# Kernel optimization log

Hardware: AMD Instinct MI355X
Metric: run time of the kernel (lower is better)

Reference implementation:

```python
import jax, jax.numpy as jnp
import numpy as np

N_NODES = 50000
N_EDGES = 262144
N_OCP = 32768
N_GRAPHS = 64
H = 128          # hidden_size
F_IN = 128       # node feature dim (== H for the stub GNN)
N_LABELS = 10


def _lin(key, fan_in, fan_out):
    return jax.random.normal(key, (fan_in, fan_out), jnp.float32) * (1.0 / float(np.sqrt(fan_in)))


def setup_inputs() -> dict:
    key = jax.random.key(0)
    ks = jax.random.split(key, 16)
    x = jax.random.normal(ks[0], (N_NODES, F_IN), jnp.float32)
    edge_index = jax.random.randint(ks[1], (2, N_EDGES), 0, N_NODES)
    batch_vec = jnp.sort(jax.random.randint(ks[2], (N_NODES,), 0, N_GRAPHS))
    y = jax.random.randint(ks[3], (N_GRAPHS,), 0, N_LABELS)
    params = {
        # stub GNN (get_node_reps): one GCN-style layer
        'W_self': _lin(ks[4], F_IN, H),
        'W_nbr': _lin(ks[5], F_IN, H),
        'b_gnn': jnp.zeros((H,), jnp.float32),
        # edge_action_rep_generator: Linear(2H,4H) ELU Linear(4H,2H) ELU Linear(2H,H)
        'Wr1': _lin(ks[6], 2 * H, 4 * H), 'br1': jnp.zeros((4 * H,), jnp.float32),
        'Wr2': _lin(ks[7], 4 * H, 2 * H), 'br2': jnp.zeros((2 * H,), jnp.float32),
        'Wr3': _lin(ks[8], 2 * H, H),     'br3': jnp.zeros((H,), jnp.float32),
        # edge_action_prob_generator: Linear(H,H) ELU Linear(H,num_labels)
        'Wp1': _lin(ks[9], H, H),         'bp1': jnp.zeros((H,), jnp.float32),
        'Wp2': _lin(ks[10], H, N_LABELS), 'bp2': jnp.zeros((N_LABELS,), jnp.float32),
    }
    return dict(x=x, edge_index=edge_index, batch_vec=batch_vec, y=y, n_ocp=N_OCP, **params)


def reference(x, edge_index, batch_vec, y, n_ocp,
              W_self, W_nbr, b_gnn,
              Wr1, br1, Wr2, br2, Wr3, br3,
              Wp1, bp1, Wp2, bp2):
    N = x.shape[0]
    G = y.shape[0]

    def get_node_reps(ei):
        # stub for self.model.get_node_reps: elu(x @ W_self + A @ (x @ W_nbr))
        msg = x[ei[0]] @ W_nbr                                   # [E', H]
        agg = jax.ops.segment_sum(msg, ei[1], num_segments=N)    # [N, H]
        return jax.nn.elu(x @ W_self + agg + b_gnn)

    ocp_edge_index = edge_index[:, :n_ocp]    # state == True edges
    ava_edge_index = edge_index[:, n_ocp:]    # state == False edges

    ava_node_reps = get_node_reps(edge_index) - get_node_reps(ocp_edge_index)  # [N, H]

    # gather per available edge + concat src/dst reps -> [E_ava, 2H]
    a = jnp.concatenate([ava_node_reps[ava_edge_index[0]],
                         ava_node_reps[ava_edge_index[1]]], axis=1)
    # edge_action_rep_generator
    a = jax.nn.elu(a @ Wr1 + br1)
    a = jax.nn.elu(a @ Wr2 + br2)
    a = a @ Wr3 + br3                                            # [E_ava, H]
    # edge_action_prob_generator
    h = jax.nn.elu(a @ Wp1 + bp1)
    logits = h @ Wp2 + bp2                                       # [E_ava, L]

    seg = batch_vec[ava_edge_index[0]]                           # graph id per ava edge
    y_edge = y[seg]                                              # target label per edge
    sel = jnp.take_along_axis(logits, y_edge[:, None], axis=1)[:, 0]  # gather(1, y)

    # segment-wise softmax over edges of each graph
    mx = jax.ops.segment_max(sel, seg, num_segments=G)
    ex = jnp.exp(sel - mx[seg])
    probs = ex / jax.ops.segment_sum(ex, seg, num_segments=G)[seg]    # [E_ava]

    # scatter_max: per-graph max prob and its argmax edge index
    pmax = jax.ops.segment_max(probs, seg, num_segments=G)            # [G]
    E = probs.shape[0]
    idx = jnp.where(probs == pmax[seg], jnp.arange(E), E)
    added_actions = jax.ops.segment_min(idx, seg, num_segments=G)     # [G]

    return probs, pmax, added_actions
```

## Files before the change

kernel.cpp:

```cpp
#include <hip/hip_runtime.h>

#define NN   50000
#define NNP  50048
#define NE   262144
#define NOCP 32768
#define EAVA (NE - NOCP)
#define NG   64
#define HD   128
#define CAP  48
#define CHNK 32768

typedef _Float16 f16x8 __attribute__((ext_vector_type(8)));
typedef _Float16 f16x2 __attribute__((ext_vector_type(2)));
typedef float f32x4 __attribute__((ext_vector_type(4)));

#define WAITVM12() asm volatile("s_waitcnt vmcnt(12)" ::: "memory")
#define WAITVM6()  asm volatile("s_waitcnt vmcnt(6)" ::: "memory")
#define WAITVM0()  asm volatile("s_waitcnt vmcnt(0)" ::: "memory")

__device__ __forceinline__ float elu_f(float v) { return v > 0.f ? v : (expf(v) - 1.f); }

__device__ __forceinline__ unsigned fenc(float f) {
  unsigned u = __float_as_uint(f);
  return (u & 0x80000000u) ? ~u : (u | 0x80000000u);
}
__device__ __forceinline__ float fdec(unsigned u) {
  return __uint_as_float((u & 0x80000000u) ? (u & 0x7fffffffu) : ~u);
}

__device__ __forceinline__ void dma16(const void* g, void* l) {
  __builtin_amdgcn_global_load_lds((const __attribute__((address_space(1))) unsigned int*)g,
                                   (__attribute__((address_space(3))) unsigned int*)l,
                                   16, 0, 0);
}

__global__ __launch_bounds__(256) void zero_i(int* __restrict__ p, int n) {
  for (int i = blockIdx.x * 256 + threadIdx.x; i < n; i += gridDim.x * 256) p[i] = 0;
}

__global__ void init_small(unsigned* mx_enc, float* denom, unsigned* pmax_enc, int* amin) {
  int t = threadIdx.x;
  if (t < NG) { mx_enc[t] = 0u; denom[t] = 0.f; pmax_enc[t] = 0u; amin[t] = EAVA; }
}

__global__ __launch_bounds__(256) void zero_tails(_Float16* __restrict__ base) {
  int t = blockIdx.x * 256 + threadIdx.x;
  if (t >= 6 * 768) return;
  int arr = t / 768, off = t % 768;
  f16x8 z = {};
  *(f16x8*)(base + (size_t)arr * NNP * HD + (size_t)NN * HD + (size_t)off * 8) = z;
}

__global__ __launch_bounds__(256) void bucket_kernel(const int* __restrict__ ei,
    int* __restrict__ cnt, int* __restrict__ bucket) {
  int e = blockIdx.x * 256 + threadIdx.x;
  if (e >= NE) return;
  int dst = ei[NE + e];
  int src = ei[e];
  int slot = atomicAdd(&cnt[dst], 1);
  if (slot < CAP)
    bucket[(size_t)dst * CAP + slot] = (int)((unsigned)src | (e < NOCP ? 0x80000000u : 0u));
}

__global__ __launch_bounds__(256) void gather_kernel(const float* __restrict__ x,
    const int* __restrict__ cnt, const int* __restrict__ bucket,
    _Float16* __restrict__ xsah, _Float16* __restrict__ xsal,
    _Float16* __restrict__ xsoh, _Float16* __restrict__ xsol) {
  int n = blockIdx.x * 4 + (threadIdx.x >> 6);
  if (n >= NN) return;
  int lane = threadIdx.x & 63;
  int c = cnt[n];
  if (c > CAP) c = CAP;
  float2 aall = make_float2(0.f, 0.f), aocp = aall;
  const int* bk = bucket + (size_t)n * CAP;
  for (int i0 = 0; i0 < c; i0 += 4) {
    int4 pk = *(const int4*)(bk + i0);
    bool m1 = (i0 + 1 < c), m2 = (i0 + 2 < c), m3 = (i0 + 3 < c);
    int r0 = pk.x & 0x7fffffff;
    int r1 = m1 ? (pk.y & 0x7fffffff) : 0;
    int r2 = m2 ? (pk.z & 0x7fffffff) : 0;
    int r3 = m3 ? (pk.w & 0x7fffffff) : 0;
    float2 v0 = *(const float2*)(x + (size_t)r0 * HD + lane * 2);
    float2 v1 = *(const float2*)(x + (size_t)r1 * HD + lane * 2);
    float2 v2 = *(const float2*)(x + (size_t)r2 * HD + lane * 2);
    float2 v3 = *(const float2*)(x + (size_t)r3 * HD + lane * 2);
    aall.x += v0.x; aall.y += v0.y;
    if (pk.x < 0) { aocp.x += v0.x; aocp.y += v0.y; }
    if (m1) { aall.x += v1.x; aall.y += v1.y; if (pk.y < 0) { aocp.x += v1.x; aocp.y += v1.y; } }
    if (m2) { aall.x += v2.x; aall.y += v2.y; if (pk.z < 0) { aocp.x += v2.x; aocp.y += v2.y; } }
    if (m3) { aall.x += v3.x; aall.y += v3.y; if (pk.w < 0) { aocp.x += v3.x; aocp.y += v3.y; } }
  }
  size_t o = (size_t)n * HD + lane * 2;
  _Float16 h0 = (_Float16)aall.x, h1 = (_Float16)aall.y;
  *(f16x2*)(xsah + o) = (f16x2){h0, h1};
  *(f16x2*)(xsal + o) = (f16x2){(_Float16)(aall.x - (float)h0), (_Float16)(aall.y - (float)h1)};
  _Float16 g0 = (_Float16)aocp.x, g1 = (_Float16)aocp.y;
  *(f16x2*)(xsoh + o) = (f16x2){g0, g1};
  *(f16x2*)(xsol + o) = (f16x2){(_Float16)(aocp.x - (float)g0), (_Float16)(aocp.y - (float)g1)};
}

__global__ __launch_bounds__(256) void split_x(const float* __restrict__ r,
    _Float16* __restrict__ rh, _Float16* __restrict__ rl) {
  int t = blockIdx.x * 256 + threadIdx.x;
  if (t >= NN * HD / 8) return;
  const float4* p = (const float4*)(r + (size_t)t * 8);
  float4 v0 = p[0], v1 = p[1];
  float vv[8] = {v0.x, v0.y, v0.z, v0.w, v1.x, v1.y, v1.z, v1.w};
  f16x8 hv, lv;
#pragma unroll
  for (int j = 0; j < 8; ++j) {
    _Float16 hh = (_Float16)vv[j];
    hv[j] = hh;
    lv[j] = (_Float16)(vv[j] - (float)hh);
  }
  *(f16x8*)(rh + (size_t)t * 8) = hv;
  *(f16x8*)(rl + (size_t)t * 8) = lv;
}

__global__ void pack_w2(const float* __restrict__ Wself, const float* __restrict__ Wnbr,
    _Float16* __restrict__ oh, _Float16* __restrict__ ol) {
  int chunk = blockIdx.x;
  int lane = threadIdx.x;
  int ns = chunk & 7, kt = chunk >> 3;
  int n = ns * 16 + (lane & 15);
  int k0 = kt * 32 + (lane >> 4) * 8;
  f16x8 hv, lv;
#pragma unroll
  for (int j = 0; j < 8; ++j) {
    int k = k0 + j;
    float v = (k < 128) ? Wself[(size_t)k * 128 + n] : Wnbr[(size_t)(k - 128) * 128 + n];
    _Float16 hh = (_Float16)v;
    hv[j] = hh;
    lv[j] = (_Float16)(v - (float)hh);
  }
  *(f16x8*)(oh + (size_t)chunk * 512 + lane * 8) = hv;
  *(f16x8*)(ol + (size_t)chunk * 512 + lane * 8) = lv;
}

__global__ void pack_w(const float* __restrict__ W, int K, int N,
    _Float16* __restrict__ oh, _Float16* __restrict__ ol) {
  int chunk = blockIdx.x;
  int lane = threadIdx.x;
  int NS = N >> 4;
  int ns = chunk % NS, kt = chunk / NS;
  int n = ns * 16 + (lane & 15);
  int k0 = kt * 32 + (lane >> 4) * 8;
  f16x8 hv, lv;
#pragma unroll
  for (int j = 0; j < 8; ++j) {
    float v = W[(size_t)(k0 + j) * N + n];
    _Float16 hh = (_Float16)v;
    hv[j] = hh;
    lv[j] = (_Float16)(v - (float)hh);
  }
  *(f16x8*)(oh + (size_t)chunk * 512 + lane * 8) = hv;
  *(f16x8*)(ol + (size_t)chunk * 512 + lane * 8) = lv;
}

__global__ void w34_kernel(const float* __restrict__ Wr3, const float* __restrict__ Wp1,
    const float* __restrict__ br3, const float* __restrict__ bp1,
    float* __restrict__ W34, float* __restrict__ b34) {
  int i = blockIdx.x, j = threadIdx.x;
  float s = 0.f;
  for (int k = 0; k < 128; ++k) s += Wr3[i * 128 + k] * Wp1[k * 128 + j];
  W34[i * 128 + j] = s;
  if (i == 0) {
    float t = bp1[j];
    for (int k = 0; k < 128; ++k) t += br3[k] * Wp1[k * 128 + j];
    b34[j] = t;
  }
}

template <int KT, int NS_B, int AMODE, int KT_NEXT, int NB>
__global__ __launch_bounds__(256) void gemm_ab(
    const _Float16* __restrict__ Ah, const _Float16* __restrict__ Al,
    const int* __restrict__ idx0, const int* __restrict__ idx1,
    const _Float16* __restrict__ Bh, const _Float16* __restrict__ Bl,
    const float* __restrict__ bias,
    _Float16* __restrict__ Oh, _Float16* __restrict__ Ol) {
  __shared__ char smem[73728] __attribute__((aligned(16)));
  float* sC = (float*)smem;

  const int tid = threadIdx.x;
  const int w = tid >> 6, lane = tid & 63;
  const int l16 = lane & 15, g16 = lane >> 4;
  const int f = blockIdx.x;
  const int r8 = f & 7;
  const int nb = (f >> 3) % NB;
  const int q8 = f / (8 * NB);
  const int bm = (q8 * 8 + r8) * 128, bn = nb * 64;
  const int w2r = w >> 1, w2c = w & 1;
  const int bmT = bm >> 4, bnS = bn >> 4;

  f32x4 acc[4][2];
#pragma unroll
  for (int i = 0; i < 4; ++i)
#pragma unroll
    for (int j = 0; j < 2; ++j) acc[i][j] = (f32x4)0.f;

  int i0a = 0, i0b = 0, i1a = 0, i1b = 0;
  if constexpr (AMODE == 1) {
    int rr0 = bm + w * 32 + l16;
    i0a = idx0[rr0]; i0b = idx0[rr0 + 16];
    i1a = idx1[rr0]; i1b = idx1[rr0 + 16];
  }

  auto STAGE = [&](int kt, int buf) {
    char* base = smem + buf * 24576;
    if constexpr (AMODE == 0) {
#pragma unroll
      for (int s = 0; s < 2; ++s) {
        int msub = w * 2 + s;
        size_t ch = (size_t)(bmT + msub) * KT + kt;
        dma16((const char*)Ah + ch * 1024 + lane * 16, base + msub * 1024);
        dma16((const char*)Al + ch * 1024 + lane * 16, base + 8192 + msub * 1024);
      }
    } else {
      int col = (kt & 3) * 32 + g16 * 8;
      int r0 = (kt < 4) ? i0a : i1a;
      int r1 = (kt < 4) ? i0b : i1b;
      dma16(Ah + (size_t)r0 * HD + col, base + (w * 2) * 1024);
      dma16(Al + (size_t)r0 * HD + col, base + 8192 + (w * 2) * 1024);
      dma16(Ah + (size_t)r1 * HD + col, base + (w * 2 + 1) * 1024);
      dma16(Al + (size_t)r1 * HD + col, base + 8192 + (w * 2 + 1) * 1024);
    }
    size_t chb = (size_t)kt * NS_B + bnS + w;
    dma16((const char*)Bh + chb * 1024 + lane * 16, base + 16384 + w * 1024);
    dma16((const char*)Bl + chb * 1024 + lane * 16, base + 20480 + w * 1024);
  };

  auto COMPUTE = [&](int buf) {
    const _Float16* sAh = (const _Float16*)(smem + buf * 24576);
    const _Float16* sAl = (const _Float16*)(smem + buf * 24576 + 8192);
    const _Float16* sBh = (const _Float16*)(smem + buf * 24576 + 16384);
    const _Float16* sBl = (const _Float16*)(smem + buf * 24576 + 20480);
    f16x8 ah[4], al[4];
#pragma unroll
    for (int mi = 0; mi < 4; ++mi) {
      ah[mi] = *(const f16x8*)(sAh + (w2r * 4 + mi) * 512 + lane * 8);
      al[mi] = *(const f16x8*)(sAl + (w2r * 4 + mi) * 512 + lane * 8);
    }
#pragma unroll
    for (int ni = 0; ni < 2; ++ni) {
      f16x8 bh = *(const f16x8*)(sBh + (w2c * 2 + ni) * 512 + lane * 8);
      f16x8 bl = *(const f16x8*)(sBl + (w2c * 2 + ni) * 512 + lane * 8);
#pragma unroll
      for (int mi = 0; mi < 4; ++mi) {
        acc[mi][ni] = __builtin_amdgcn_mfma_f32_16x16x32_f16(ah[mi], bh, acc[mi][ni], 0, 0, 0);
        acc[mi][ni] = __builtin_amdgcn_mfma_f32_16x16x32_f16(al[mi], bh, acc[mi][ni], 0, 0, 0);
        acc[mi][ni] = __builtin_amdgcn_mfma_f32_16x16x32_f16(ah[mi], bl, acc[mi][ni], 0, 0, 0);
      }
    }
  };

  STAGE(0, 0);
  STAGE(1, 1);
#pragma unroll
  for (int kt = 0; kt < KT; ++kt) {
    if (kt + 2 < KT) STAGE(kt + 2, (kt + 2) % 3);
    if (kt < KT - 2) WAITVM12();
    else if (kt == KT - 2) WAITVM6();
    else WAITVM0();
    __builtin_amdgcn_s_barrier();
    COMPUTE(kt % 3);
    __builtin_amdgcn_s_barrier();
  }

#pragma unroll
  for (int ni = 0; ni < 2; ++ni) {
    int colL = (w2c * 2 + ni) * 16 + l16;
    float bv = bias[bn + colL];
#pragma unroll
    for (int mi = 0; mi < 4; ++mi) {
      int rowb = w2r * 64 + mi * 16 + g16 * 4;
#pragma unroll
      for (int r = 0; r < 4; ++r)
        sC[(rowb + r) * 68 + colL] = elu_f(acc[mi][ni][r] + bv);
    }
  }
  __syncthreads();
  const int bnT32 = bn >> 5;
#pragma unroll
  for (int c = 0; c < 4; ++c) {
    int chunkid = w * 4 + c;
    int msub = chunkid >> 1, ktl = chunkid & 1;
    int m = msub * 16 + l16;
    int cb = ktl * 32 + g16 * 8;
    f16x8 hv, lv;
#pragma unroll
    for (int j = 0; j < 8; ++j) {
      float v = sC[m * 68 + cb + j];
      _Float16 hh = (_Float16)v;
      hv[j] = hh;
      lv[j] = (_Float16)(v - (float)hh);
    }
    size_t gchunk = (size_t)(bmT + msub) * KT_NEXT + (bnT32 + ktl);
    *(f16x8*)((char*)Oh + gchunk * 1024 + lane * 16) = hv;
    *(f16x8*)((char*)Ol + gchunk * 1024 + lane * 16) = lv;
  }
}

__global__ __launch_bounds__(64) void reps_direct(
    const _Float16* __restrict__ xh, const _Float16* __restrict__ xl,
    const _Float16* __restrict__ xsah, const _Float16* __restrict__ xsal,
    const _Float16* __restrict__ xsoh, const _Float16* __restrict__ xsol,
    const _Float16* __restrict__ Wsh, const _Float16* __restrict__ Wsl,
    const float* __restrict__ bias,
    _Float16* __restrict__ Oh, _Float16* __restrict__ Ol) {
  __shared__ float sC[64][68];
  const int lane = threadIdx.x;
  const int mt = blockIdx.x, nt = blockIdx.y;
  const int bm = mt * 64, bn = nt * 64;
  const int l16 = lane & 15, g16 = lane >> 4;

  f32x4 acc1[4][4], acc2[4][4];
#pragma unroll
  for (int i = 0; i < 4; ++i)
#pragma unroll
    for (int j = 0; j < 4; ++j) acc1[i][j] = (f32x4)0.f;

  auto CP3 = [&](f32x4 (*acc)[4], const f16x8* ah, const f16x8* al,
                 const f16x8* bh, const f16x8* bl) {
#pragma unroll
    for (int ni = 0; ni < 4; ++ni)
#pragma unroll
      for (int mi = 0; mi < 4; ++mi) {
        acc[mi][ni] = __builtin_amdgcn_mfma_f32_16x16x32_f16(ah[mi], bh[ni], acc[mi][ni], 0, 0, 0);
        acc[mi][ni] = __builtin_amdgcn_mfma_f32_16x16x32_f16(al[mi], bh[ni], acc[mi][ni], 0, 0, 0);
        acc[mi][ni] = __builtin_amdgcn_mfma_f32_16x16x32_f16(ah[mi], bl[ni], acc[mi][ni], 0, 0, 0);
      }
  };

#pragma unroll
  for (int kt = 0; kt < 4; ++kt) {
    f16x8 ah[4], al[4], bh[4], bl[4];
#pragma unroll
    for (int mi = 0; mi < 4; ++mi) {
      size_t off = (size_t)(bm + mi * 16 + l16) * HD + kt * 32 + g16 * 8;
      ah[mi] = *(const f16x8*)(xh + off);
      al[mi] = *(const f16x8*)(xl + off);
    }
#pragma unroll
    for (int ni = 0; ni < 4; ++ni) {
      size_t ch = (size_t)kt * 8 + nt * 4 + ni;
      bh[ni] = *(const f16x8*)(Wsh + ch * 512 + lane * 8);
      bl[ni] = *(const f16x8*)(Wsl + ch * 512 + lane * 8);
    }
    CP3(acc1, ah, al, bh, bl);
  }
#pragma unroll
  for (int i = 0; i < 4; ++i)
#pragma unroll
    for (int j = 0; j < 4; ++j) acc2[i][j] = acc1[i][j];

#pragma unroll
  for (int kt = 0; kt < 4; ++kt) {
    f16x8 aah[4], aal[4], aoh[4], aol[4], bh[4], bl[4];
#pragma unroll
    for (int mi = 0; mi < 4; ++mi) {
      size_t off = (size_t)(bm + mi * 16 + l16) * HD + kt * 32 + g16 * 8;
      aah[mi] = *(const f16x8*)(xsah + off);
      aal[mi] = *(const f16x8*)(xsal + off);
      aoh[mi] = *(const f16x8*)(xsoh + off);
      aol[mi] = *(const f16x8*)(xsol + off);
    }
#pragma unroll
    for (int ni = 0; ni < 4; ++ni) {
      size_t ch = (size_t)(kt + 4) * 8 + nt * 4 + ni;
      bh[ni] = *(const f16x8*)(Wsh + ch * 512 + lane * 8);
      bl[ni] = *(const f16x8*)(Wsl + ch * 512 + lane * 8);
    }
    CP3(acc1, aah, aal, bh, bl);
    CP3(acc2, aoh, aol, bh, bl);
  }

#pragma unroll
  for (int ni = 0; ni < 4; ++ni) {
    int colL = ni * 16 + l16;
    float bv = bias[bn + colL];
#pragma unroll
    for (int mi = 0; mi < 4; ++mi) {
      int rowb = mi * 16 + g16 * 4;
#pragma unroll
      for (int r = 0; r < 4; ++r)
        sC[rowb + r][colL] = elu_f(acc1[mi][ni][r] + bv) - elu_f(acc2[mi][ni][r] + bv);
    }
  }
  __syncthreads();
#pragma unroll
  for (int c = 0; c < 8; ++c) {
    int msub = c >> 1, ktl = c & 1;
    int m = msub * 16 + l16;
    int cb = ktl * 32 + g16 * 8;
    int grow = bm + m;
    if (grow < NN) {
      f16x8 hv, lv;
#pragma unroll
      for (int j = 0; j < 8; ++j) {
        float v = sC[m][cb + j];
        _Float16 hh = (_Float16)v;
        hv[j] = hh;
        lv[j] = (_Float16)(v - (float)hh);
      }
      *(f16x8*)(Oh + (size_t)grow * HD + bn + cb) = hv;
      *(f16x8*)(Ol + (size_t)grow * HD + bn + cb) = lv;
    }
  }
}

__global__ __launch_bounds__(256) void gemm3_sel(
    const _Float16* __restrict__ Ah, const _Float16* __restrict__ Al,
    const _Float16* __restrict__ Bh, const _Float16* __restrict__ Bl,
    const float* __restrict__ b34,
    const int* __restrict__ ei, const int* __restrict__ batchv, const int* __restrict__ yv,
    const float* __restrict__ Wp2, const float* __restrict__ bp2,
    float* __restrict__ sel, int* __restrict__ seg, int co) {
  __shared__ char smem[73728] __attribute__((aligned(16)));
  const int tid = threadIdx.x;
  const int w = tid >> 6, lane = tid & 63;
  const int l16 = lane & 15, g16 = lane >> 4;
  const int mt = blockIdx.x;

  f32x4 acc[8];
#pragma unroll
  for (int j = 0; j < 8; ++j) acc[j] = (f32x4)0.f;

  auto STAGE = [&](int kt, int buf) {
    char* base = smem + buf * 24576;
    size_t ch = (size_t)(mt * 4 + w) * 8 + kt;
    dma16((const char*)Ah + ch * 1024 + lane * 16, base + w * 1024);
    dma16((const char*)Al + ch * 1024 + lane * 16, base + 4096 + w * 1024);
#pragma unroll
    for (int s = 0; s < 2; ++s) {
      int nsub = w * 2 + s;
      size_t chb = (size_t)kt * 8 + nsub;
      dma16((const char*)Bh + chb * 1024 + lane * 16, base + 8192 + nsub * 1024);
      dma16((const char*)Bl + chb * 1024 + lane * 16, base + 16384 + nsub * 1024);
    }
  };

  auto COMPUTE = [&](int buf) {
    const _Float16* sAh = (const _Float16*)(smem + buf * 24576);
    const _Float16* sAl = (const _Float16*)(smem + buf * 24576 + 4096);
    const _Float16* sBh = (const _Float16*)(smem + buf * 24576 + 8192);
    const _Float16* sBl = (const _Float16*)(smem + buf * 24576 + 16384);
    f16x8 ah = *(const f16x8*)(sAh + w * 512 + lane * 8);
    f16x8 al = *(const f16x8*)(sAl + w * 512 + lane * 8);
#pragma unroll
    for (int ni = 0; ni < 8; ++ni) {
      f16x8 bh = *(const f16x8*)(sBh + ni * 512 + lane * 8);
      f16x8 bl = *(const f16x8*)(sBl + ni * 512 + lane * 8);
      acc[ni] = __builtin_amdgcn_mfma_f32_16x16x32_f16(ah, bh, acc[ni], 0, 0, 0);
      acc[ni] = __builtin_amdgcn_mfma_f32_16x16x32_f16(al, bh, acc[ni], 0, 0, 0);
      acc[ni] = __builtin_amdgcn_mfma_f32_16x16x32_f16(ah, bl, acc[ni], 0, 0, 0);
    }
  };

  STAGE(0, 0);
  STAGE(1, 1);
#pragma unroll
  for (int kt = 0; kt < 8; ++kt) {
    if (kt + 2 < 8) STAGE(kt + 2, (kt + 2) % 3);
    if (kt < 6) WAITVM12();
    else if (kt == 6) WAITVM6();
    else WAITVM0();
    __builtin_amdgcn_s_barrier();
    COMPUTE(kt % 3);
    __builtin_amdgcn_s_barrier();
  }

  float bb[8];
#pragma unroll
  for (int ni = 0; ni < 8; ++ni) bb[ni] = b34[ni * 16 + l16];

#pragma unroll
  for (int rr = 0; rr < 4; ++rr) {
    int row = w * 16 + g16 * 4 + rr;
    int e = co + mt * 64 + row;
    int s = ei[NOCP + e];
    int gg = batchv[s];
    int c = yv[gg];
    float a = 0.f;
#pragma unroll
    for (int ni = 0; ni < 8; ++ni)
      a += elu_f(acc[ni][rr] + bb[ni]) * Wp2[(ni * 16 + l16) * 10 + c];
    a += __shfl_xor(a, 1);
    a += __shfl_xor(a, 2);
    a += __shfl_xor(a, 4);
    a += __shfl_xor(a, 8);
    if (l16 == 0) { sel[e] = a + bp2[c]; seg[e] = gg; }
  }
}

__global__ __launch_bounds__(256) void segmax_sel(const float* __restrict__ sel,
    const int* __restrict__ seg, unsigned* __restrict__ mx_enc) {
  __shared__ unsigned sm[NG];
  int tid = threadIdx.x;
  if (tid < NG) sm[tid] = 0u;
  __syncthreads();
  for (int i = blockIdx.x * blockDim.x + tid; i < EAVA; i += gridDim.x * blockDim.x)
    atomicMax(&sm[seg[i]], fenc(sel[i]));
  __syncthreads();
  if (tid < NG) atomicMax(&mx_enc[tid], sm[tid]);
}

__global__ __launch_bounds__(256) void exden_kernel(const float* __restrict__ sel,
    const int* __restrict__ seg, const unsigned* __restrict__ mx_enc,
    float* __restrict__ denom, float* __restrict__ out_probs) {
  __shared__ float sd[NG];
  __shared__ float smx[NG];
  int tid = threadIdx.x;
  if (tid < NG) { smx[tid] = fdec(mx_enc[tid]); sd[tid] = 0.f; }
  __syncthreads();
  for (int i = blockIdx.x * blockDim.x + tid; i < EAVA; i += gridDim.x * blockDim.x) {
    int g = seg[i];
    float ex = expf(sel[i] - smx[g]);
    out_probs[i] = ex;
    atomicAdd(&sd[g], ex);
  }
  __syncthreads();
  if (tid < NG) atomicAdd(&denom[tid], sd[tid]);
}

__global__ __launch_bounds__(256) void probpmax_kernel(const int* __restrict__ seg,
    const float* __restrict__ denom, float* __restrict__ out_probs,
    unsigned* __restrict__ pmax_enc) {
  __shared__ float sden[NG];
  __shared__ unsigned sp[NG];
  int tid = threadIdx.x;
  if (tid < NG) { sden[tid] = denom[tid]; sp[tid] = 0u; }
  __syncthreads();
  for (int i = blockIdx.x * blockDim.x + tid; i < EAVA; i += gridDim.x * blockDim.x) {
    int g = seg[i];
    float p = out_probs[i] / sden[g];
    out_probs[i] = p;
    atomicMax(&sp[g], fenc(p));
  }
  __syncthreads();
  if (tid < NG) atomicMax(&pmax_enc[tid], sp[tid]);
}

__global__ __launch_bounds__(256) void argmin_kernel(const int* __restrict__ seg,
    const float* __restrict__ out_probs, const unsigned* __restrict__ pmax_enc,
    int* __restrict__ amin) {
  __shared__ float spm[NG];
  __shared__ int sa[NG];
  int tid = threadIdx.x;
  if (tid < NG) { spm[tid] = fdec(pmax_enc[tid]); sa[tid] = EAVA; }
  __syncthreads();
  for (int i = blockIdx.x * blockDim.x + tid; i < EAVA; i += gridDim.x * blockDim.x) {
    int g = seg[i];
    if (out_probs[i] == spm[g]) atomicMin(&sa[g], i);
  }
  __syncthreads();
  if (tid < NG) atomicMin(&amin[tid], sa[tid]);
}

__global__ void finalize_kernel(const unsigned* __restrict__ pmax_enc,
    const int* __restrict__ amin, float* __restrict__ out) {
  int g = threadIdx.x;
  if (g < NG) {
    out[EAVA + g] = fdec(pmax_enc[g]);
    out[EAVA + NG + g] = (float)amin[g];
  }
}

extern "C" void kernel_launch(void* const* d_in, const int* in_sizes, int n_in,
                              void* d_out, int out_size, void* d_ws, size_t ws_size,
                              hipStream_t stream) {
  const float* x      = (const float*)d_in[0];
  const int*   ei     = (const int*)d_in[1];
  const int*   batchv = (const int*)d_in[2];
  const int*   yv     = (const int*)d_in[3];
  const float* Wself = (const float*)d_in[5];
  const float* Wnbr  = (const float*)d_in[6];
  const float* bgnn  = (const float*)d_in[7];
  const float* Wr1   = (const float*)d_in[8];
  const float* br1   = (const float*)d_in[9];
  const float* Wr2   = (const float*)d_in[10];
  const float* br2   = (const float*)d_in[11];
  const float* Wr3   = (const float*)d_in[12];
  const float* br3   = (const float*)d_in[13];
  const float* Wp1   = (const float*)d_in[14];
  const float* bp1   = (const float*)d_in[15];
  const float* Wp2   = (const float*)d_in[16];
  const float* bp2   = (const float*)d_in[17];
  float* out = (float*)d_out;

  char* wp = (char*)d_ws;
  auto alloc = [&](size_t bytes) -> char* {
    char* p = wp;
    wp += (bytes + 255) & ~(size_t)255;
    return p;
  };
  _Float16* xsplit = (_Float16*)alloc((size_t)6 * NNP * HD * 2);
  _Float16* xh   = xsplit + (size_t)0 * NNP * HD;
  _Float16* xl   = xsplit + (size_t)1 * NNP * HD;
  _Float16* xsah = xsplit + (size_t)2 * NNP * HD;
  _Float16* xsal = xsplit + (size_t)3 * NNP * HD;
  _Float16* xsoh = xsplit + (size_t)4 * NNP * HD;
  _Float16* xsol = xsplit + (size_t)5 * NNP * HD;
  _Float16*  reps_h   = (_Float16*)alloc((size_t)NN * HD * 2);
  _Float16*  reps_l   = (_Float16*)alloc((size_t)NN * HD * 2);
  int*       cnt      = (int*)alloc((size_t)NN * 4);
  int*       bucket   = (int*)alloc((size_t)NN * CAP * 4);
  float*     sel      = (float*)alloc((size_t)EAVA * 4);
  int*       seg      = (int*)alloc((size_t)EAVA * 4);
  unsigned*  mx_enc   = (unsigned*)alloc(NG * 4);
  float*     denom    = (float*)alloc(NG * 4);
  unsigned*  pmax_enc = (unsigned*)alloc(NG * 4);
  int*       amin     = (int*)alloc(NG * 4);
  _Float16*  Wsh  = (_Float16*)alloc((size_t)64 * 1024);
  _Float16*  Wsl  = (_Float16*)alloc((size_t)64 * 1024);
  _Float16*  Wr1h = (_Float16*)alloc((size_t)8 * 32 * 1024);
  _Float16*  Wr1l = (_Float16*)alloc((size_t)8 * 32 * 1024);
  _Float16*  Wr2h = (_Float16*)alloc((size_t)16 * 16 * 1024);
  _Float16*  Wr2l = (_Float16*)alloc((size_t)16 * 16 * 1024);
  float*     W34  = (float*)alloc((size_t)256 * 128 * 4);
  float*     b34  = (float*)alloc(128 * 4);
  _Float16*  W34h = (_Float16*)alloc((size_t)8 * 8 * 1024);
  _Float16*  W34l = (_Float16*)alloc((size_t)8 * 8 * 1024);
  _Float16*  b1h = (_Float16*)alloc((size_t)(CHNK / 16) * 16 * 1024);
  _Float16*  b1l = (_Float16*)alloc((size_t)(CHNK / 16) * 16 * 1024);
  _Float16*  b2h = (_Float16*)alloc((size_t)(CHNK / 16) * 8 * 1024);
  _Float16*  b2l = (_Float16*)alloc((size_t)(CHNK / 16) * 8 * 1024);
  (void)ws_size;

  zero_i<<<64, 256, 0, stream>>>(cnt, NN);
  init_small<<<1, 64, 0, stream>>>(mx_enc, denom, pmax_enc, amin);
  zero_tails<<<18, 256, 0, stream>>>(xsplit);
  bucket_kernel<<<NE / 256, 256, 0, stream>>>(ei, cnt, bucket);
  gather_kernel<<<(NN + 3) / 4, 256, 0, stream>>>(x, cnt, bucket, xsah, xsal, xsoh, xsol);
  split_x<<<(NN * HD / 8 + 255) / 256, 256, 0, stream>>>(x, xh, xl);
  pack_w2<<<64, 64, 0, stream>>>(Wself, Wnbr, Wsh, Wsl);
  reps_direct<<<dim3(NNP / 64, 2), 64, 0, stream>>>(xh, xl, xsah, xsal, xsoh, xsol, Wsh, Wsl,
                                                    bgnn, reps_h, reps_l);
  w34_kernel<<<256, 128, 0, stream>>>(Wr3, Wp1, br3, bp1, W34, b34);
  pack_w<<<8 * 32, 64, 0, stream>>>(Wr1, 256, 512, Wr1h, Wr1l);
  pack_w<<<16 * 16, 64, 0, stream>>>(Wr2, 512, 256, Wr2h, Wr2l);
  pack_w<<<8 * 8, 64, 0, stream>>>(W34, 256, 128, W34h, W34l);

  for (int c = 0; c < 7; ++c) {
    int co = c * CHNK;
    gemm_ab<8, 32, 1, 16, 8><<<2048, 256, 0, stream>>>(
        reps_h, reps_l, ei + NOCP + co, ei + NE + NOCP + co, Wr1h, Wr1l, br1, b1h, b1l);
    gemm_ab<16, 16, 0, 8, 4><<<1024, 256, 0, stream>>>(
        b1h, b1l, nullptr, nullptr, Wr2h, Wr2l, br2, b2h, b2l);
    gemm3_sel<<<CHNK / 64, 256, 0, stream>>>(
        b2h, b2l, W34h, W34l, b34, ei, batchv, yv, Wp2, bp2, sel, seg, co);
  }

  segmax_sel<<<112, 256, 0, stream>>>(sel, seg, mx_enc);
  exden_kernel<<<112, 256, 0, stream>>>(sel, seg, mx_enc, denom, out);
  probpmax_kernel<<<112, 256, 0, stream>>>(seg, denom, out, pmax_enc);
  argmin_kernel<<<112, 256, 0, stream>>>(seg, out, pmax_enc, amin);
  finalize_kernel<<<1, 64, 0, stream>>>(pmax_enc, amin, out);
}
```

Before: 924.6 us.

## Process all available edges in one MLP pass when workspace allows; halve reps tile

When the workspace is large enough, the edge MLP runs as three single launches over all available edges instead of seven chunked rounds of three launches. Intermediate buffers grow to full size, trading memory traffic that may spill out of cache for fewer launches and tail effects. The reps_direct kernel also uses 32-row tiles instead of 64, doubling its grid for better occupancy at the cost of reloading weights per block.

```diff
diff --git a/kernel.cpp b/kernel.cpp
--- a/kernel.cpp
+++ b/kernel.cpp
@@ -307,15 +307,15 @@
     const _Float16* __restrict__ Wsh, const _Float16* __restrict__ Wsl,
     const float* __restrict__ bias,
     _Float16* __restrict__ Oh, _Float16* __restrict__ Ol) {
-  __shared__ float sC[64][68];
+  __shared__ float sC[32][68];
   const int lane = threadIdx.x;
   const int mt = blockIdx.x, nt = blockIdx.y;
-  const int bm = mt * 64, bn = nt * 64;
+  const int bm = mt * 32, bn = nt * 64;
   const int l16 = lane & 15, g16 = lane >> 4;
 
-  f32x4 acc1[4][4], acc2[4][4];
-#pragma unroll
-  for (int i = 0; i < 4; ++i)
+  f32x4 acc1[2][4], acc2[2][4];
+#pragma unroll
+  for (int i = 0; i < 2; ++i)
 #pragma unroll
     for (int j = 0; j < 4; ++j) acc1[i][j] = (f32x4)0.f;
 
@@ -324,7 +324,7 @@
 #pragma unroll
     for (int ni = 0; ni < 4; ++ni)
 #pragma unroll
-      for (int mi = 0; mi < 4; ++mi) {
+      for (int mi = 0; mi < 2; ++mi) {
         acc[mi][ni] = __builtin_amdgcn_mfma_f32_16x16x32_f16(ah[mi], bh[ni], acc[mi][ni], 0, 0, 0);
         acc[mi][ni] = __builtin_amdgcn_mfma_f32_16x16x32_f16(al[mi], bh[ni], acc[mi][ni], 0, 0, 0);
         acc[mi][ni] = __builtin_amdgcn_mfma_f32_16x16x32_f16(ah[mi], bl[ni], acc[mi][ni], 0, 0, 0);
@@ -333,9 +333,9 @@
 
 #pragma unroll
   for (int kt = 0; kt < 4; ++kt) {
-    f16x8 ah[4], al[4], bh[4], bl[4];
-#pragma unroll
-    for (int mi = 0; mi < 4; ++mi) {
+    f16x8 ah[2], al[2], bh[4], bl[4];
+#pragma unroll
+    for (int mi = 0; mi < 2; ++mi) {
       size_t off = (size_t)(bm + mi * 16 + l16) * HD + kt * 32 + g16 * 8;
       ah[mi] = *(const f16x8*)(xh + off);
       al[mi] = *(const f16x8*)(xl + off);
@@ -349,15 +349,15 @@
     CP3(acc1, ah, al, bh, bl);
   }
 #pragma unroll
-  for (int i = 0; i < 4; ++i)
+  for (int i = 0; i < 2; ++i)
 #pragma unroll
     for (int j = 0; j < 4; ++j) acc2[i][j] = acc1[i][j];
 
 #pragma unroll
   for (int kt = 0; kt < 4; ++kt) {
-    f16x8 aah[4], aal[4], aoh[4], aol[4], bh[4], bl[4];
-#pragma unroll
-    for (int mi = 0; mi < 4; ++mi) {
+    f16x8 aah[2], aal[2], aoh[2], aol[2], bh[4], bl[4];
+#pragma unroll
+    for (int mi = 0; mi < 2; ++mi) {
       size_t off = (size_t)(bm + mi * 16 + l16) * HD + kt * 32 + g16 * 8;
       aah[mi] = *(const f16x8*)(xsah + off);
       aal[mi] = *(const f16x8*)(xsal + off);
@@ -379,7 +379,7 @@
     int colL = ni * 16 + l16;
     float bv = bias[bn + colL];
 #pragma unroll
-    for (int mi = 0; mi < 4; ++mi) {
+    for (int mi = 0; mi < 2; ++mi) {
       int rowb = mi * 16 + g16 * 4;
 #pragma unroll
       for (int r = 0; r < 4; ++r)
@@ -388,7 +388,7 @@
   }
   __syncthreads();
 #pragma unroll
-  for (int c = 0; c < 8; ++c) {
+  for (int c = 0; c < 4; ++c) {
     int msub = c >> 1, ktl = c & 1;
     int m = msub * 16 + l16;
     int cb = ktl * 32 + g16 * 8;
@@ -620,10 +620,24 @@
   float*     b34  = (float*)alloc(128 * 4);
   _Float16*  W34h = (_Float16*)alloc((size_t)8 * 8 * 1024);
   _Float16*  W34l = (_Float16*)alloc((size_t)8 * 8 * 1024);
-  _Float16*  b1h = (_Float16*)alloc((size_t)(CHNK / 16) * 16 * 1024);
-  _Float16*  b1l = (_Float16*)alloc((size_t)(CHNK / 16) * 16 * 1024);
-  _Float16*  b2h = (_Float16*)alloc((size_t)(CHNK / 16) * 8 * 1024);
-  _Float16*  b2l = (_Float16*)alloc((size_t)(CHNK / 16) * 8 * 1024);
+
+  const size_t b1_full = (size_t)(EAVA / 16) * 16 * 1024;
+  const size_t b2_full = (size_t)(EAVA / 16) * 8 * 1024;
+  size_t used = (size_t)(wp - (char*)d_ws);
+  bool full = ws_size >= used + 2 * b1_full + 2 * b2_full + (1u << 20);
+
+  _Float16 *b1h, *b1l, *b2h, *b2l;
+  if (full) {
+    b1h = (_Float16*)alloc(b1_full);
+    b1l = (_Float16*)alloc(b1_full);
+    b2h = (_Float16*)alloc(b2_full);
+    b2l = (_Float16*)alloc(b2_full);
+  } else {
+    b1h = (_Float16*)alloc((size_t)(CHNK / 16) * 16 * 1024);
+    b1l = (_Float16*)alloc((size_t)(CHNK / 16) * 16 * 1024);
+    b2h = (_Float16*)alloc((size_t)(CHNK / 16) * 8 * 1024);
+    b2l = (_Float16*)alloc((size_t)(CHNK / 16) * 8 * 1024);
+  }
   (void)ws_size;
 
   zero_i<<<64, 256, 0, stream>>>(cnt, NN);
@@ -633,21 +647,30 @@
   gather_kernel<<<(NN + 3) / 4, 256, 0, stream>>>(x, cnt, bucket, xsah, xsal, xsoh, xsol);
   split_x<<<(NN * HD / 8 + 255) / 256, 256, 0, stream>>>(x, xh, xl);
   pack_w2<<<64, 64, 0, stream>>>(Wself, Wnbr, Wsh, Wsl);
-  reps_direct<<<dim3(NNP / 64, 2), 64, 0, stream>>>(xh, xl, xsah, xsal, xsoh, xsol, Wsh, Wsl,
+  reps_direct<<<dim3(NNP / 32, 2), 64, 0, stream>>>(xh, xl, xsah, xsal, xsoh, xsol, Wsh, Wsl,
                                                     bgnn, reps_h, reps_l);
   w34_kernel<<<256, 128, 0, stream>>>(Wr3, Wp1, br3, bp1, W34, b34);
   pack_w<<<8 * 32, 64, 0, stream>>>(Wr1, 256, 512, Wr1h, Wr1l);
   pack_w<<<16 * 16, 64, 0, stream>>>(Wr2, 512, 256, Wr2h, Wr2l);
   pack_w<<<8 * 8, 64, 0, stream>>>(W34, 256, 128, W34h, W34l);
 
-  for (int c = 0; c < 7; ++c) {
-    int co = c * CHNK;
-    gemm_ab<8, 32, 1, 16, 8><<<2048, 256, 0, stream>>>(
-        reps_h, reps_l, ei + NOCP + co, ei + NE + NOCP + co, Wr1h, Wr1l, br1, b1h, b1l);
-    gemm_ab<16, 16, 0, 8, 4><<<1024, 256, 0, stream>>>(
+  if (full) {
+    gemm_ab<8, 32, 1, 16, 8><<<(EAVA / 128) * 8, 256, 0, stream>>>(
+        reps_h, reps_l, ei + NOCP, ei + NE + NOCP, Wr1h, Wr1l, br1, b1h, b1l);
+    gemm_ab<16, 16, 0, 8, 4><<<(EAVA / 128) * 4, 256, 0, stream>>>(
         b1h, b1l, nullptr, nullptr, Wr2h, Wr2l, br2, b2h, b2l);
-    gemm3_sel<<<CHNK / 64, 256, 0, stream>>>(
-        b2h, b2l, W34h, W34l, b34, ei, batchv, yv, Wp2, bp2, sel, seg, co);
+    gemm3_sel<<<EAVA / 64, 256, 0, stream>>>(
+        b2h, b2l, W34h, W34l, b34, ei, batchv, yv, Wp2, bp2, sel, seg, 0);
+  } else {
+    for (int c = 0; c < 7; ++c) {
+      int co = c * CHNK;
+      gemm_ab<8, 32, 1, 16, 8><<<(CHNK / 128) * 8, 256, 0, stream>>>(
+          reps_h, reps_l, ei + NOCP + co, ei + NE + NOCP + co, Wr1h, Wr1l, br1, b1h, b1l);
+      gemm_ab<16, 16, 0, 8, 4><<<(CHNK / 128) * 4, 256, 0, stream>>>(
+          b1h, b1l, nullptr, nullptr, Wr2h, Wr2l, br2, b2h, b2l);
+      gemm3_sel<<<CHNK / 64, 256, 0, stream>>>(
+          b2h, b2l, W34h, W34l, b34, ei, batchv, yv, Wp2, bp2, sel, seg, co);
+    }
   }
 
   segmax_sel<<<112, 256, 0, stream>>>(sel, seg, mx_enc);
```

Result: no change. 907.0 us (-1.9%).

## Halve GEMM M-tile to 64 rows and switch to double-buffered LDS pipeline

Applied to the files above, without the earlier changes.

The gemm_ab kernel's M tile shrinks from 128 to 64 rows, each wave now covers 16 rows, the LDS footprint drops from 72KB to 32KB, and the triple-buffer prefetch becomes a double buffer with a single-stage lookahead. reps_direct likewise halves its row tile to 32 and launches twice as many blocks. The aim is higher occupancy and more blocks per launch, with better latency hiding on the gather-heavy GEMMs. The cost is less B-operand reuse per loaded tile, more B traffic overall, and a shallower prefetch depth.

```diff
diff --git a/kernel.cpp b/kernel.cpp
--- a/kernel.cpp
+++ b/kernel.cpp
@@ -16,6 +16,7 @@
 
 #define WAITVM12() asm volatile("s_waitcnt vmcnt(12)" ::: "memory")
 #define WAITVM6()  asm volatile("s_waitcnt vmcnt(6)" ::: "memory")
+#define WAITVM4()  asm volatile("s_waitcnt vmcnt(4)" ::: "memory")
 #define WAITVM0()  asm volatile("s_waitcnt vmcnt(0)" ::: "memory")
 
 __device__ __forceinline__ float elu_f(float v) { return v > 0.f ? v : (expf(v) - 1.f); }
@@ -178,7 +179,7 @@
     const _Float16* __restrict__ Bh, const _Float16* __restrict__ Bl,
     const float* __restrict__ bias,
     _Float16* __restrict__ Oh, _Float16* __restrict__ Ol) {
-  __shared__ char smem[73728] __attribute__((aligned(16)));
+  __shared__ char smem[32768] __attribute__((aligned(16)));
   float* sC = (float*)smem;
 
   const int tid = threadIdx.x;
@@ -188,64 +189,57 @@
   const int r8 = f & 7;
   const int nb = (f >> 3) % NB;
   const int q8 = f / (8 * NB);
-  const int bm = (q8 * 8 + r8) * 128, bn = nb * 64;
+  const int bm = (q8 * 8 + r8) * 64, bn = nb * 64;
   const int w2r = w >> 1, w2c = w & 1;
   const int bmT = bm >> 4, bnS = bn >> 4;
 
-  f32x4 acc[4][2];
-#pragma unroll
-  for (int i = 0; i < 4; ++i)
+  f32x4 acc[2][2];
+#pragma unroll
+  for (int i = 0; i < 2; ++i)
 #pragma unroll
     for (int j = 0; j < 2; ++j) acc[i][j] = (f32x4)0.f;
 
-  int i0a = 0, i0b = 0, i1a = 0, i1b = 0;
+  int i0w = 0, i1w = 0;
   if constexpr (AMODE == 1) {
-    int rr0 = bm + w * 32 + l16;
-    i0a = idx0[rr0]; i0b = idx0[rr0 + 16];
-    i1a = idx1[rr0]; i1b = idx1[rr0 + 16];
+    int rr = bm + w * 16 + l16;
+    i0w = idx0[rr];
+    i1w = idx1[rr];
   }
 
   auto STAGE = [&](int kt, int buf) {
-    char* base = smem + buf * 24576;
+    char* base = smem + buf * 16384;
     if constexpr (AMODE == 0) {
-#pragma unroll
-      for (int s = 0; s < 2; ++s) {
-        int msub = w * 2 + s;
-        size_t ch = (size_t)(bmT + msub) * KT + kt;
-        dma16((const char*)Ah + ch * 1024 + lane * 16, base + msub * 1024);
-        dma16((const char*)Al + ch * 1024 + lane * 16, base + 8192 + msub * 1024);
-      }
+      size_t ch = (size_t)(bmT + w) * KT + kt;
+      dma16((const char*)Ah + ch * 1024 + lane * 16, base + w * 1024);
+      dma16((const char*)Al + ch * 1024 + lane * 16, base + 4096 + w * 1024);
     } else {
       int col = (kt & 3) * 32 + g16 * 8;
-      int r0 = (kt < 4) ? i0a : i1a;
-      int r1 = (kt < 4) ? i0b : i1b;
-      dma16(Ah + (size_t)r0 * HD + col, base + (w * 2) * 1024);
-      dma16(Al + (size_t)r0 * HD + col, base + 8192 + (w * 2) * 1024);
-      dma16(Ah + (size_t)r1 * HD + col, base + (w * 2 + 1) * 1024);
-      dma16(Al + (size_t)r1 * HD + col, base + 8192 + (w * 2 + 1) * 1024);
+      int r = (kt < 4) ? i0w : i1w;
+      dma16(Ah + (size_t)r * HD + col, base + w * 1024);
+      dma16(Al + (size_t)r * HD + col, base + 4096 + w * 1024);
     }
     size_t chb = (size_t)kt * NS_B + bnS + w;
-    dma16((const char*)Bh + chb * 1024 + lane * 16, base + 16384 + w * 1024);
-    dma16((const char*)Bl + chb * 1024 + lane * 16, base + 20480 + w * 1024);
+    dma16((const char*)Bh + chb * 1024 + lane * 16, base + 8192 + w * 1024);
+    dma16((const char*)Bl + chb * 1024 + lane * 16, base + 12288 + w * 1024);
   };
 
   auto COMPUTE = [&](int buf) {
-    const _Float16* sAh = (const _Float16*)(smem + buf * 24576);
-    const _Float16* sAl = (const _Float16*)(smem + buf * 24576 + 8192);
-    const _Float16* sBh = (const _Float16*)(smem + buf * 24576 + 16384);
-    const _Float16* sBl = (const _Float16*)(smem + buf * 24576 + 20480);
-    f16x8 ah[4], al[4];
-#pragma unroll
-    for (int mi = 0; mi < 4; ++mi) {
-      ah[mi] = *(const f16x8*)(sAh + (w2r * 4 + mi) * 512 + lane * 8);
-      al[mi] = *(const f16x8*)(sAl + (w2r * 4 + mi) * 512 + lane * 8);
+    const _Float16* sAh = (const _Float16*)(smem + buf * 16384);
+    const _Float16* sAl = (const _Float16*)(smem + buf * 16384 + 4096);
+    const _Float16* sBh = (const _Float16*)(smem + buf * 16384 + 8192);
+    const _Float16* sBl = (const _Float16*)(smem + buf * 16384 + 12288);
+    f16x8 ah[2], al[2];
+#pragma unroll
+    for (int mi = 0; mi < 2; ++mi) {
+      ah[mi] = *(const f16x8*)(sAh + (w2r * 2 + mi) * 512 + lane * 8);
+      al[mi] = *(const f16x8*)(sAl + (w2r * 2 + mi) * 512 + lane * 8);
     }
 #pragma unroll
     for (int ni = 0; ni < 2; ++ni) {
       f16x8 bh = *(const f16x8*)(sBh + (w2c * 2 + ni) * 512 + lane * 8);
       f16x8 bl = *(const f16x8*)(sBl + (w2c * 2 + ni) * 512 + lane * 8);
 #pragma unroll
-      for (int mi = 0; mi < 4; ++mi) {
+      for (int mi = 0; mi < 2; ++mi) {
         acc[mi][ni] = __builtin_amdgcn_mfma_f32_16x16x32_f16(ah[mi], bh, acc[mi][ni], 0, 0, 0);
         acc[mi][ni] = __builtin_amdgcn_mfma_f32_16x16x32_f16(al[mi], bh, acc[mi][ni], 0, 0, 0);
         acc[mi][ni] = __builtin_amdgcn_mfma_f32_16x16x32_f16(ah[mi], bl, acc[mi][ni], 0, 0, 0);
@@ -254,15 +248,16 @@
   };
 
   STAGE(0, 0);
-  STAGE(1, 1);
 #pragma unroll
   for (int kt = 0; kt < KT; ++kt) {
-    if (kt + 2 < KT) STAGE(kt + 2, (kt + 2) % 3);
-    if (kt < KT - 2) WAITVM12();
-    else if (kt == KT - 2) WAITVM6();
-    else WAITVM0();
+    if (kt + 1 < KT) {
+      STAGE(kt + 1, (kt + 1) & 1);
+      WAITVM4();
+    } else {
+      WAITVM0();
+    }
     __builtin_amdgcn_s_barrier();
-    COMPUTE(kt % 3);
+    COMPUTE(kt & 1);
     __builtin_amdgcn_s_barrier();
   }
 
@@ -271,8 +266,8 @@
     int colL = (w2c * 2 + ni) * 16 + l16;
     float bv = bias[bn + colL];
 #pragma unroll
-    for (int mi = 0; mi < 4; ++mi) {
-      int rowb = w2r * 64 + mi * 16 + g16 * 4;
+    for (int mi = 0; mi < 2; ++mi) {
+      int rowb = w2r * 32 + mi * 16 + g16 * 4;
 #pragma unroll
       for (int r = 0; r < 4; ++r)
         sC[(rowb + r) * 68 + colL] = elu_f(acc[mi][ni][r] + bv);
@@ -281,8 +276,8 @@
   __syncthreads();
   const int bnT32 = bn >> 5;
 #pragma unroll
-  for (int c = 0; c < 4; ++c) {
-    int chunkid = w * 4 + c;
+  for (int s = 0; s < 2; ++s) {
+    int chunkid = w * 2 + s;
     int msub = chunkid >> 1, ktl = chunkid & 1;
     int m = msub * 16 + l16;
     int cb = ktl * 32 + g16 * 8;
@@ -307,15 +302,15 @@
     const _Float16* __restrict__ Wsh, const _Float16* __restrict__ Wsl,
     const float* __restrict__ bias,
     _Float16* __restrict__ Oh, _Float16* __restrict__ Ol) {
-  __shared__ float sC[64][68];
+  __shared__ float sC[32][68];
   const int lane = threadIdx.x;
   const int mt = blockIdx.x, nt = blockIdx.y;
-  const int bm = mt * 64, bn = nt * 64;
+  const int bm = mt * 32, bn = nt * 64;
   const int l16 = lane & 15, g16 = lane >> 4;
 
-  f32x4 acc1[4][4], acc2[4][4];
-#pragma unroll
-  for (int i = 0; i < 4; ++i)
+  f32x4 acc1[2][4], acc2[2][4];
+#pragma unroll
+  for (int i = 0; i < 2; ++i)
 #pragma unroll
     for (int j = 0; j < 4; ++j) acc1[i][j] = (f32x4)0.f;
 
@@ -324,7 +319,7 @@
 #pragma unroll
     for (int ni = 0; ni < 4; ++ni)
 #pragma unroll
-      for (int mi = 0; mi < 4; ++mi) {
+      for (int mi = 0; mi < 2; ++mi) {
         acc[mi][ni] = __builtin_amdgcn_mfma_f32_16x16x32_f16(ah[mi], bh[ni], acc[mi][ni], 0, 0, 0);
         acc[mi][ni] = __builtin_amdgcn_mfma_f32_16x16x32_f16(al[mi], bh[ni], acc[mi][ni], 0, 0, 0);
         acc[mi][ni] = __builtin_amdgcn_mfma_f32_16x16x32_f16(ah[mi], bl[ni], acc[mi][ni], 0, 0, 0);
@@ -333,9 +328,9 @@
 
 #pragma unroll
   for (int kt = 0; kt < 4; ++kt) {
-    f16x8 ah[4], al[4], bh[4], bl[4];
-#pragma unroll
-    for (int mi = 0; mi < 4; ++mi) {
+    f16x8 ah[2], al[2], bh[4], bl[4];
+#pragma unroll
+    for (int mi = 0; mi < 2; ++mi) {
       size_t off = (size_t)(bm + mi * 16 + l16) * HD + kt * 32 + g16 * 8;
       ah[mi] = *(const f16x8*)(xh + off);
       al[mi] = *(const f16x8*)(xl + off);
@@ -349,15 +344,15 @@
     CP3(acc1, ah, al, bh, bl);
   }
 #pragma unroll
-  for (int i = 0; i < 4; ++i)
+  for (int i = 0; i < 2; ++i)
 #pragma unroll
     for (int j = 0; j < 4; ++j) acc2[i][j] = acc1[i][j];
 
 #pragma unroll
   for (int kt = 0; kt < 4; ++kt) {
-    f16x8 aah[4], aal[4], aoh[4], aol[4], bh[4], bl[4];
-#pragma unroll
-    for (int mi = 0; mi < 4; ++mi) {
+    f16x8 aah[2], aal[2], aoh[2], aol[2], bh[4], bl[4];
+#pragma unroll
+    for (int mi = 0; mi < 2; ++mi) {
       size_t off = (size_t)(bm + mi * 16 + l16) * HD + kt * 32 + g16 * 8;
       aah[mi] = *(const f16x8*)(xsah + off);
       aal[mi] = *(const f16x8*)(xsal + off);
@@ -379,7 +374,7 @@
     int colL = ni * 16 + l16;
     float bv = bias[bn + colL];
 #pragma unroll
-    for (int mi = 0; mi < 4; ++mi) {
+    for (int mi = 0; mi < 2; ++mi) {
       int rowb = mi * 16 + g16 * 4;
 #pragma unroll
       for (int r = 0; r < 4; ++r)
@@ -388,7 +383,7 @@
   }
   __syncthreads();
 #pragma unroll
-  for (int c = 0; c < 8; ++c) {
+  for (int c = 0; c < 4; ++c) {
     int msub = c >> 1, ktl = c & 1;
     int m = msub * 16 + l16;
     int cb = ktl * 32 + g16 * 8;
@@ -633,7 +628,7 @@
   gather_kernel<<<(NN + 3) / 4, 256, 0, stream>>>(x, cnt, bucket, xsah, xsal, xsoh, xsol);
   split_x<<<(NN * HD / 8 + 255) / 256, 256, 0, stream>>>(x, xh, xl);
   pack_w2<<<64, 64, 0, stream>>>(Wself, Wnbr, Wsh, Wsl);
-  reps_direct<<<dim3(NNP / 64, 2), 64, 0, stream>>>(xh, xl, xsah, xsal, xsoh, xsol, Wsh, Wsl,
+  reps_direct<<<dim3(NNP / 32, 2), 64, 0, stream>>>(xh, xl, xsah, xsal, xsoh, xsol, Wsh, Wsl,
                                                     bgnn, reps_h, reps_l);
   w34_kernel<<<256, 128, 0, stream>>>(Wr3, Wp1, br3, bp1, W34, b34);
   pack_w<<<8 * 32, 64, 0, stream>>>(Wr1, 256, 512, Wr1h, Wr1l);
@@ -642,9 +637,9 @@
 
   for (int c = 0; c < 7; ++c) {
     int co = c * CHNK;
-    gemm_ab<8, 32, 1, 16, 8><<<2048, 256, 0, stream>>>(
+    gemm_ab<8, 32, 1, 16, 8><<<(CHNK / 64) * 8, 256, 0, stream>>>(
         reps_h, reps_l, ei + NOCP + co, ei + NE + NOCP + co, Wr1h, Wr1l, br1, b1h, b1l);
-    gemm_ab<16, 16, 0, 8, 4><<<1024, 256, 0, stream>>>(
+    gemm_ab<16, 16, 0, 8, 4><<<(CHNK / 64) * 4, 256, 0, stream>>>(
         b1h, b1l, nullptr, nullptr, Wr2h, Wr2l, br2, b2h, b2l);
     gemm3_sel<<<CHNK / 64, 256, 0, stream>>>(
         b2h, b2l, W34h, W34l, b34, ei, batchv, yv, Wp2, bp2, sel, seg, co);
```

Result: no change. 931.6 us (+0.8%).
